# Kernel optimization log

Measured on AMD Instinct MI355X. Metric: run time of the kernel, lower is better.

The kernel has to match this reference:

```python
import jax, jax.numpy as jnp
import numpy as np

N_NODES = 50000
N_EDGES = 800000
IN_DIM = 128
HID = 128
N_LAYERS = 2


def setup_inputs() -> dict:
    key = jax.random.key(0)
    ks = jax.random.split(key, 16)
    x = jax.random.normal(ks[0], (N_NODES, IN_DIM), dtype=jnp.float32)
    edge_index = jax.random.randint(ks[1], (2, N_EDGES), 0, N_NODES, dtype=jnp.int64)
    def lin(k, fan_in, fan_out):
        bound = 1.0 / np.sqrt(fan_in)
        k1, k2 = jax.random.split(k)
        W = jax.random.uniform(k1, (fan_in, fan_out), jnp.float32, -bound, bound)
        b = jax.random.uniform(k2, (fan_out,), jnp.float32, -bound, bound)
        return W, b
    W1_0, b1_0 = lin(ks[2], IN_DIM, HID)
    W2_0, b2_0 = lin(ks[3], HID, HID)
    W1_1, b1_1 = lin(ks[4], HID, HID)
    W2_1, b2_1 = lin(ks[5], HID, HID)
    Wr, br = lin(ks[6], HID, 1)
    return dict(x=x, edge_index=edge_index,
                W1_0=W1_0, b1_0=b1_0, W2_0=W2_0, b2_0=b2_0,
                W1_1=W1_1, b1_1=b1_1, W2_1=W2_1, b2_1=b2_1,
                Wr=Wr, br=br)


def _gin_conv(x, src, dst, W1, b1, W2, b2):
    # GINConv (eps=0): h = MLP(x + sum_{j in N(i)} x_j)
    msgs = x[src]                                   # [E, d] gather
    agg = jax.ops.segment_sum(msgs, dst, num_segments=x.shape[0])  # [N, d] scatter-add
    h = x + agg
    h = jax.nn.relu(h @ W1 + b1)
    return h @ W2 + b2


def reference(x, edge_index, W1_0, b1_0, W2_0, b2_0, W1_1, b1_1, W2_1, b2_1, Wr, br):
    src, dst = edge_index[0], edge_index[1]
    # layer 0
    h = jax.nn.relu(_gin_conv(x, src, dst, W1_0, b1_0, W2_0, b2_0))
    # layer 1 (dropout is identity in eval mode)
    h = jax.nn.relu(_gin_conv(h, src, dst, W1_1, b1_1, W2_1, b2_1))
    return h @ Wr + br
```

## Files before the change

kernel.cpp:

```cpp
#include <hip/hip_runtime.h>

#define HIDDEN 128
#define NB_SHIFT 7
#define NPB 128
#define EPB 4096

typedef __attribute__((ext_vector_type(8))) short short8;
typedef __attribute__((ext_vector_type(4))) float f32x4;
typedef _Float16 f16;
typedef __attribute__((ext_vector_type(8))) _Float16 f16x8;

__device__ __forceinline__ ushort f2bf(float a) {
  union { float f; unsigned u; } c; c.f = a;
  return (ushort)((c.u + 0x7FFFu + ((c.u >> 16) & 1u)) >> 16);
}
__device__ __forceinline__ float bf2f(ushort h) {
  union { unsigned u; float f; } c; c.u = ((unsigned)h) << 16;
  return c.f;
}

__global__ __launch_bounds__(256) void bucket_hist_kernel(
    const int* __restrict__ dst, int* __restrict__ bcnt, int E, int NB) {
  __shared__ int loc[512];
  const int t = threadIdx.x;
  loc[t] = 0; loc[t + 256] = 0;
  __syncthreads();
  const int base = blockIdx.x * EPB;
  const int end = min(base + EPB, E);
  for (int e = base + t; e < end; e += 256)
    atomicAdd(&loc[dst[e] >> NB_SHIFT], 1);
  __syncthreads();
  for (int b = t; b < NB; b += 256)
    if (loc[b]) atomicAdd(&bcnt[b], loc[b]);
}

__global__ __launch_bounds__(256) void scan_buckets_kernel(
    const int* __restrict__ bcnt, int* __restrict__ pairOff,
    int* __restrict__ gCursor, int NB) {
  __shared__ int sh[512];
  const int t = threadIdx.x;
  const int v0 = (t < NB) ? bcnt[t] : 0;
  const int v1 = (t + 256 < NB) ? bcnt[t + 256] : 0;
  sh[t] = v0; sh[t + 256] = v1;
  __syncthreads();
#pragma unroll
  for (int off = 1; off < 512; off <<= 1) {
    int a = (t >= off) ? sh[t - off] : 0;
    int b = (t + 256 >= off) ? sh[t + 256 - off] : 0;
    __syncthreads();
    sh[t] += a; sh[t + 256] += b;
    __syncthreads();
  }
  const int e0 = sh[t] - v0;
  const int e1 = sh[t + 256] - v1;
  pairOff[t] = e0; gCursor[t] = e0;
  pairOff[t + 256] = e1; gCursor[t + 256] = e1;
  if (t == 255) pairOff[512] = sh[511];
}

__global__ __launch_bounds__(256) void partition_kernel(
    const int* __restrict__ src, const int* __restrict__ dst,
    int* __restrict__ gCursor, int* __restrict__ pairs, int E, int NB) {
  __shared__ int loc[512];
  __shared__ int cur[512];
  const int t = threadIdx.x;
  loc[t] = 0; loc[t + 256] = 0;
  __syncthreads();
  const int base = blockIdx.x * EPB;
  const int end = min(base + EPB, E);
  for (int e = base + t; e < end; e += 256)
    atomicAdd(&loc[dst[e] >> NB_SHIFT], 1);
  __syncthreads();
  for (int b = t; b < NB; b += 256)
    cur[b] = loc[b] ? atomicAdd(&gCursor[b], loc[b]) : 0;
  __syncthreads();
  for (int e = base + t; e < end; e += 256) {
    const int d = dst[e];
    const int p = atomicAdd(&cur[d >> NB_SHIFT], 1);
    pairs[p] = ((d & (NPB - 1)) << 25) | src[e];
  }
}

__global__ __launch_bounds__(256) void build_csr_kernel(
    const int* __restrict__ pairs, const int* __restrict__ pairOff,
    int* __restrict__ rowptr, int* __restrict__ col, int M, int E, int NB) {
  __shared__ int deg[NPB];
  __shared__ int pre[NPB];
  __shared__ int cur[NPB];
  const int b = blockIdx.x;
  const int t = threadIdx.x;
  const int s = pairOff[b];
  const int e2 = pairOff[b + 1];
  const int nodeBase = b << NB_SHIFT;
  const int nNodes = min(NPB, M - nodeBase);
  if (t < NPB) deg[t] = 0;
  __syncthreads();
  for (int i = s + t; i < e2; i += 256)
    atomicAdd(&deg[((unsigned)pairs[i]) >> 25], 1);
  __syncthreads();
  if (t < NPB) pre[t] = deg[t];
  __syncthreads();
#pragma unroll
  for (int off = 1; off < NPB; off <<= 1) {
    int v = (t < NPB && t >= off) ? pre[t - off] : 0;
    __syncthreads();
    if (t < NPB) pre[t] += v;
    __syncthreads();
  }
  if (t < nNodes) rowptr[nodeBase + t] = s + pre[t] - deg[t];
  if (b == NB - 1 && t == 0) rowptr[M] = E;
  if (t < NPB) cur[t] = pre[t] - deg[t];
  __syncthreads();
  for (int i = s + t; i < e2; i += 256) {
    const int pr = pairs[i];
    const int pos = s + atomicAdd(&cur[((unsigned)pr) >> 25], 1);
    col[pos] = pr & 0x1FFFFFF;
  }
}

__global__ __launch_bounds__(256) void f2h_kernel(const float* __restrict__ in,
                                                  f16* __restrict__ out, int n8) {
  int i = blockIdx.x * 256 + threadIdx.x;
  if (i >= n8) return;
  const float4* p = (const float4*)(in + (size_t)i * 8);
  float4 a = p[0], b = p[1];
  f16x8 o;
  o[0] = (f16)a.x; o[1] = (f16)a.y; o[2] = (f16)a.z; o[3] = (f16)a.w;
  o[4] = (f16)b.x; o[5] = (f16)b.y; o[6] = (f16)b.z; o[7] = (f16)b.w;
  *(f16x8*)(out + (size_t)i * 8) = o;
}

__global__ __launch_bounds__(256) void prepack_kernel(
    const float* __restrict__ Wa, const float* __restrict__ Wb,
    const float* __restrict__ Wc, const float* __restrict__ Wd,
    ushort* __restrict__ out) {
  int idx = blockIdx.x * 256 + threadIdx.x;
  int w = idx >> 11;
  int rem = idx & 2047;
  int ks = rem >> 9;
  int nf = (rem >> 6) & 7;
  int lane = rem & 63;
  const float* W = (w == 0) ? Wa : (w == 1) ? Wb : (w == 2) ? Wc : Wd;
  const int kbase = ks * 32 + (lane >> 4) * 8;
  const int n = nf * 16 + (lane & 15);
  ushort* oh = out + (size_t)w * 32768 + (size_t)rem * 8;
  ushort* ol = oh + 16384;
#pragma unroll
  for (int j = 0; j < 8; ++j) {
    float v = W[(size_t)(kbase + j) * HIDDEN + n];
    ushort h = f2bf(v);
    oh[j] = h;
    ol[j] = f2bf(v - bf2f(h));
  }
}

__global__ __launch_bounds__(256, 4) void gin_layer_kernel(
    const f16* __restrict__ xh, const int* __restrict__ rowptr,
    const int* __restrict__ col, const ushort* __restrict__ W1p,
    const float* __restrict__ b1, const ushort* __restrict__ W2p,
    const float* __restrict__ b2, f16* __restrict__ Ch,
    const float* __restrict__ Wr, const float* __restrict__ br,
    float* __restrict__ outv, int M, int doReadout) {
  __shared__ float h1[4][16][133];
  const int t = threadIdx.x;
  const int lane = t & 63;
  const int w = t >> 6;
  const int r = lane & 15;
  const int g = lane >> 4;
  const int mBase = blockIdx.x * 64 + w * 16;
  int arow = mBase + r;
  if (arow > M - 1) arow = M - 1;

  float a32[4][8];
  {
    const f16* rp = xh + (size_t)arow * HIDDEN + g * 8;
    f16x8 s0 = *(const f16x8*)(rp);
    f16x8 s1 = *(const f16x8*)(rp + 32);
    f16x8 s2 = *(const f16x8*)(rp + 64);
    f16x8 s3 = *(const f16x8*)(rp + 96);
#pragma unroll
    for (int j = 0; j < 8; ++j) {
      a32[0][j] = (float)s0[j]; a32[1][j] = (float)s1[j];
      a32[2][j] = (float)s2[j]; a32[3][j] = (float)s3[j];
    }
    const int s = rowptr[arow];
    const int e = rowptr[arow + 1];
    int i = s;
    for (; i + 3 < e; i += 4) {
      const int c0 = col[i], c1 = col[i + 1], c2 = col[i + 2], c3 = col[i + 3];
      const f16* p0 = xh + (size_t)c0 * HIDDEN + g * 8;
      const f16* p1 = xh + (size_t)c1 * HIDDEN + g * 8;
      const f16* p2 = xh + (size_t)c2 * HIDDEN + g * 8;
      const f16* p3 = xh + (size_t)c3 * HIDDEN + g * 8;
      f16x8 u0 = *(const f16x8*)(p0);
      f16x8 u1 = *(const f16x8*)(p0 + 32);
      f16x8 u2 = *(const f16x8*)(p0 + 64);
      f16x8 u3 = *(const f16x8*)(p0 + 96);
      f16x8 v0 = *(const f16x8*)(p1);
      f16x8 v1 = *(const f16x8*)(p1 + 32);
      f16x8 v2 = *(const f16x8*)(p1 + 64);
      f16x8 v3 = *(const f16x8*)(p1 + 96);
      f16x8 w0 = *(const f16x8*)(p2);
      f16x8 w1 = *(const f16x8*)(p2 + 32);
      f16x8 w2 = *(const f16x8*)(p2 + 64);
      f16x8 w3 = *(const f16x8*)(p2 + 96);
      f16x8 x0 = *(const f16x8*)(p3);
      f16x8 x1 = *(const f16x8*)(p3 + 32);
      f16x8 x2 = *(const f16x8*)(p3 + 64);
      f16x8 x3 = *(const f16x8*)(p3 + 96);
#pragma unroll
      for (int j = 0; j < 8; ++j) {
        a32[0][j] += ((float)u0[j] + (float)v0[j]) + ((float)w0[j] + (float)x0[j]);
        a32[1][j] += ((float)u1[j] + (float)v1[j]) + ((float)w1[j] + (float)x1[j]);
        a32[2][j] += ((float)u2[j] + (float)v2[j]) + ((float)w2[j] + (float)x2[j]);
        a32[3][j] += ((float)u3[j] + (float)v3[j]) + ((float)w3[j] + (float)x3[j]);
      }
    }
    for (; i < e; ++i) {
      const int c0 = col[i];
      const f16* p0 = xh + (size_t)c0 * HIDDEN + g * 8;
      f16x8 u0 = *(const f16x8*)(p0);
      f16x8 u1 = *(const f16x8*)(p0 + 32);
      f16x8 u2 = *(const f16x8*)(p0 + 64);
      f16x8 u3 = *(const f16x8*)(p0 + 96);
#pragma unroll
      for (int j = 0; j < 8; ++j) {
        a32[0][j] += (float)u0[j];
        a32[1][j] += (float)u1[j];
        a32[2][j] += (float)u2[j];
        a32[3][j] += (float)u3[j];
      }
    }
  }

  f32x4 acc[8];
#pragma unroll
  for (int i = 0; i < 8; ++i) acc[i] = (f32x4){0.f, 0.f, 0.f, 0.f};

#pragma unroll
  for (int ks = 0; ks < 4; ++ks) {
    short8 ah, al;
#pragma unroll
    for (int j = 0; j < 8; ++j) {
      ushort h = f2bf(a32[ks][j]);
      ah[j] = (short)h;
      al[j] = (short)f2bf(a32[ks][j] - bf2f(h));
    }
#pragma unroll
    for (int nf = 0; nf < 8; ++nf) {
      const ushort* bp = W1p + ((size_t)(ks * 8 + nf) * 64 + lane) * 8;
      short8 bh = *(const short8*)bp;
      short8 bl = *(const short8*)(bp + 16384);
      acc[nf] = __builtin_amdgcn_mfma_f32_16x16x32_bf16(ah, bh, acc[nf], 0, 0, 0);
      acc[nf] = __builtin_amdgcn_mfma_f32_16x16x32_bf16(al, bh, acc[nf], 0, 0, 0);
      acc[nf] = __builtin_amdgcn_mfma_f32_16x16x32_bf16(ah, bl, acc[nf], 0, 0, 0);
    }
  }

#pragma unroll
  for (int nf = 0; nf < 8; ++nf) {
    float bv = b1[nf * 16 + r];
#pragma unroll
    for (int q = 0; q < 4; ++q)
      h1[w][g * 4 + q][nf * 16 + r] = fmaxf(acc[nf][q] + bv, 0.f);
    acc[nf] = (f32x4){0.f, 0.f, 0.f, 0.f};
  }

#pragma unroll
  for (int ks = 0; ks < 4; ++ks) {
    const float* hp = &h1[w][r][ks * 32 + g * 8];
    float4 a0 = *(const float4*)hp;
    float4 a1 = *(const float4*)(hp + 4);
    float av[8] = {a0.x, a0.y, a0.z, a0.w, a1.x, a1.y, a1.z, a1.w};
    short8 ah, al;
#pragma unroll
    for (int j = 0; j < 8; ++j) {
      ushort h = f2bf(av[j]);
      ah[j] = (short)h;
      al[j] = (short)f2bf(av[j] - bf2f(h));
    }
#pragma unroll
    for (int nf = 0; nf < 8; ++nf) {
      const ushort* bp = W2p + ((size_t)(ks * 8 + nf) * 64 + lane) * 8;
      short8 bh = *(const short8*)bp;
      short8 bl = *(const short8*)(bp + 16384);
      acc[nf] = __builtin_amdgcn_mfma_f32_16x16x32_bf16(ah, bh, acc[nf], 0, 0, 0);
      acc[nf] = __builtin_amdgcn_mfma_f32_16x16x32_bf16(al, bh, acc[nf], 0, 0, 0);
      acc[nf] = __builtin_amdgcn_mfma_f32_16x16x32_bf16(ah, bl, acc[nf], 0, 0, 0);
    }
  }

  if (!doReadout) {
#pragma unroll
    for (int nf = 0; nf < 8; ++nf) {
      float bv = b2[nf * 16 + r];
#pragma unroll
      for (int q = 0; q < 4; ++q)
        h1[w][g * 4 + q][nf * 16 + r] = fmaxf(acc[nf][q] + bv, 0.f);
    }
    const int rr = lane >> 2;
    const int c0 = (lane & 3) * 32;
    const int gm = mBase + rr;
    if (gm < M) {
#pragma unroll
      for (int i = 0; i < 4; ++i) {
        float4 v0 = *(const float4*)&h1[w][rr][c0 + i * 8];
        float4 v1 = *(const float4*)&h1[w][rr][c0 + i * 8 + 4];
        f16x8 o;
        o[0] = (f16)v0.x; o[1] = (f16)v0.y; o[2] = (f16)v0.z; o[3] = (f16)v0.w;
        o[4] = (f16)v1.x; o[5] = (f16)v1.y; o[6] = (f16)v1.z; o[7] = (f16)v1.w;
        *(f16x8*)(Ch + (size_t)gm * HIDDEN + c0 + i * 8) = o;
      }
    }
  } else {
    float p[4] = {0.f, 0.f, 0.f, 0.f};
#pragma unroll
    for (int nf = 0; nf < 8; ++nf) {
      float bv = b2[nf * 16 + r];
      float wv = Wr[nf * 16 + r];
#pragma unroll
      for (int q = 0; q < 4; ++q) {
        float h = fmaxf(acc[nf][q] + bv, 0.f);
        p[q] += h * wv;
      }
    }
#pragma unroll
    for (int q = 0; q < 4; ++q) {
      p[q] += __shfl_xor(p[q], 8);
      p[q] += __shfl_xor(p[q], 4);
      p[q] += __shfl_xor(p[q], 2);
      p[q] += __shfl_xor(p[q], 1);
    }
    if (r == 0) {
      float brv = br[0];
#pragma unroll
      for (int q = 0; q < 4; ++q) {
        int gm = mBase + g * 4 + q;
        if (gm < M) outv[gm] = p[q] + brv;
      }
    }
  }
}

extern "C" void kernel_launch(void* const* d_in, const int* in_sizes, int n_in,
                              void* d_out, int out_size, void* d_ws,
                              size_t ws_size, hipStream_t stream) {
  const float* x = (const float*)d_in[0];
  const int* ei = (const int*)d_in[1];
  const float* W1_0 = (const float*)d_in[2];
  const float* b1_0 = (const float*)d_in[3];
  const float* W2_0 = (const float*)d_in[4];
  const float* b2_0 = (const float*)d_in[5];
  const float* W1_1 = (const float*)d_in[6];
  const float* b1_1 = (const float*)d_in[7];
  const float* W2_1 = (const float*)d_in[8];
  const float* b2_1 = (const float*)d_in[9];
  const float* Wr = (const float*)d_in[10];
  const float* br = (const float*)d_in[11];

  const int M = in_sizes[0] / HIDDEN;
  const int E = in_sizes[1] / 2;
  const int* src = ei;
  const int* dst = ei + E;
  const int NB = (M + NPB - 1) >> NB_SHIFT;

  int* pairs = (int*)d_ws;
  f16* xh = (f16*)(pairs + E);
  f16* Bh = xh + (size_t)M * HIDDEN;
  int* rowptr = (int*)(Bh + (size_t)M * HIDDEN);
  int* col = rowptr + M + 1;
  int* bcnt = col + E;
  int* pairOff = bcnt + 512;
  int* gCursor = pairOff + 513;
  ushort* Wpk = (ushort*)(gCursor + 512);

  const int ginBlocks = (M + 63) / 64;
  const int cvtBlocks = (M * 16 + 255) / 256;
  const int edgeBlocks = (E + EPB - 1) / EPB;
  float* out = (float*)d_out;

  prepack_kernel<<<32, 256, 0, stream>>>(W1_0, W2_0, W1_1, W2_1, Wpk);
  f2h_kernel<<<cvtBlocks, 256, 0, stream>>>(x, xh, M * 16);

  hipMemsetAsync(bcnt, 0, 512 * sizeof(int), stream);
  bucket_hist_kernel<<<edgeBlocks, 256, 0, stream>>>(dst, bcnt, E, NB);
  scan_buckets_kernel<<<1, 256, 0, stream>>>(bcnt, pairOff, gCursor, NB);
  partition_kernel<<<edgeBlocks, 256, 0, stream>>>(src, dst, gCursor, pairs,
                                                   E, NB);
  build_csr_kernel<<<NB, 256, 0, stream>>>(pairs, pairOff, rowptr, col, M, E,
                                           NB);

  gin_layer_kernel<<<ginBlocks, 256, 0, stream>>>(
      xh, rowptr, col, Wpk, b1_0, Wpk + 32768, b2_0, Bh,
      nullptr, nullptr, nullptr, M, 0);

  gin_layer_kernel<<<ginBlocks, 256, 0, stream>>>(
      Bh, rowptr, col, Wpk + 65536, b1_1, Wpk + 98304, b2_1, nullptr,
      Wr, br, out, M, 1);
}
```

Measured before the change: 254.7 us.

## Split each node's neighbor gather and MLP output columns across two waves

Each block now handles 16 nodes with two wavefronts. Each wave gathers half of every node's neighbor list, the partial sums are combined through shared memory, and each wave then computes half of the output columns of both MLP matmuls. The goal is shorter per-wave gather latency chains and more parallelism in the memory-bound aggregation. The cost is extra syncthreads, LDS exchange traffic, and a cross-wave reduction for the readout.

```diff
diff --git a/kernel.cpp b/kernel.cpp
--- a/kernel.cpp
+++ b/kernel.cpp
@@ -154,25 +154,26 @@
   }
 }
 
-__global__ __launch_bounds__(256, 4) void gin_layer_kernel(
+__global__ __launch_bounds__(128, 6) void gin_layer_kernel(
     const f16* __restrict__ xh, const int* __restrict__ rowptr,
     const int* __restrict__ col, const ushort* __restrict__ W1p,
     const float* __restrict__ b1, const ushort* __restrict__ W2p,
     const float* __restrict__ b2, f16* __restrict__ Ch,
     const float* __restrict__ Wr, const float* __restrict__ br,
     float* __restrict__ outv, int M, int doReadout) {
-  __shared__ float h1[4][16][133];
+  __shared__ float buf[16][132];
+  __shared__ float pr[16];
   const int t = threadIdx.x;
   const int lane = t & 63;
-  const int w = t >> 6;
+  const int h = t >> 6;
   const int r = lane & 15;
   const int g = lane >> 4;
-  const int mBase = blockIdx.x * 64 + w * 16;
+  const int mBase = blockIdx.x * 16;
   int arow = mBase + r;
   if (arow > M - 1) arow = M - 1;
 
   float a32[4][8];
-  {
+  if (h == 0) {
     const f16* rp = xh + (size_t)arow * HIDDEN + g * 8;
     f16x8 s0 = *(const f16x8*)(rp);
     f16x8 s1 = *(const f16x8*)(rp + 32);
@@ -183,8 +184,18 @@
       a32[0][j] = (float)s0[j]; a32[1][j] = (float)s1[j];
       a32[2][j] = (float)s2[j]; a32[3][j] = (float)s3[j];
     }
-    const int s = rowptr[arow];
-    const int e = rowptr[arow + 1];
+  } else {
+#pragma unroll
+    for (int ks = 0; ks < 4; ++ks)
+#pragma unroll
+      for (int j = 0; j < 8; ++j) a32[ks][j] = 0.f;
+  }
+  {
+    const int sAll = rowptr[arow];
+    const int eAll = rowptr[arow + 1];
+    const int mid = sAll + ((eAll - sAll) >> 1);
+    const int s = h ? mid : sAll;
+    const int e = h ? eAll : mid;
     int i = s;
     for (; i + 3 < e; i += 4) {
       const int c0 = col[i], c1 = col[i + 1], c2 = col[i + 2], c3 = col[i + 3];
@@ -233,95 +244,142 @@
     }
   }
 
-  f32x4 acc[8];
-#pragma unroll
-  for (int i = 0; i < 8; ++i) acc[i] = (f32x4){0.f, 0.f, 0.f, 0.f};
+  if (h == 1) {
+#pragma unroll
+    for (int ks = 0; ks < 4; ++ks) {
+      *(float4*)&buf[r][ks * 32 + g * 8] =
+          make_float4(a32[ks][0], a32[ks][1], a32[ks][2], a32[ks][3]);
+      *(float4*)&buf[r][ks * 32 + g * 8 + 4] =
+          make_float4(a32[ks][4], a32[ks][5], a32[ks][6], a32[ks][7]);
+    }
+  }
+  __syncthreads();
+  if (h == 0) {
+#pragma unroll
+    for (int ks = 0; ks < 4; ++ks) {
+      float4 q0 = *(const float4*)&buf[r][ks * 32 + g * 8];
+      float4 q1 = *(const float4*)&buf[r][ks * 32 + g * 8 + 4];
+      a32[ks][0] += q0.x; a32[ks][1] += q0.y; a32[ks][2] += q0.z; a32[ks][3] += q0.w;
+      a32[ks][4] += q1.x; a32[ks][5] += q1.y; a32[ks][6] += q1.z; a32[ks][7] += q1.w;
+    }
+  }
+  __syncthreads();
+  if (h == 0) {
+#pragma unroll
+    for (int ks = 0; ks < 4; ++ks) {
+      *(float4*)&buf[r][ks * 32 + g * 8] =
+          make_float4(a32[ks][0], a32[ks][1], a32[ks][2], a32[ks][3]);
+      *(float4*)&buf[r][ks * 32 + g * 8 + 4] =
+          make_float4(a32[ks][4], a32[ks][5], a32[ks][6], a32[ks][7]);
+    }
+  }
+  __syncthreads();
+  if (h == 1) {
+#pragma unroll
+    for (int ks = 0; ks < 4; ++ks) {
+      float4 q0 = *(const float4*)&buf[r][ks * 32 + g * 8];
+      float4 q1 = *(const float4*)&buf[r][ks * 32 + g * 8 + 4];
+      a32[ks][0] = q0.x; a32[ks][1] = q0.y; a32[ks][2] = q0.z; a32[ks][3] = q0.w;
+      a32[ks][4] = q1.x; a32[ks][5] = q1.y; a32[ks][6] = q1.z; a32[ks][7] = q1.w;
+    }
+  }
+  __syncthreads();
+
+  f32x4 acc[4];
+#pragma unroll
+  for (int i = 0; i < 4; ++i) acc[i] = (f32x4){0.f, 0.f, 0.f, 0.f};
 
 #pragma unroll
   for (int ks = 0; ks < 4; ++ks) {
     short8 ah, al;
 #pragma unroll
     for (int j = 0; j < 8; ++j) {
-      ushort h = f2bf(a32[ks][j]);
-      ah[j] = (short)h;
-      al[j] = (short)f2bf(a32[ks][j] - bf2f(h));
-    }
-#pragma unroll
-    for (int nf = 0; nf < 8; ++nf) {
-      const ushort* bp = W1p + ((size_t)(ks * 8 + nf) * 64 + lane) * 8;
+      ushort hh = f2bf(a32[ks][j]);
+      ah[j] = (short)hh;
+      al[j] = (short)f2bf(a32[ks][j] - bf2f(hh));
+    }
+#pragma unroll
+    for (int nfi = 0; nfi < 4; ++nfi) {
+      const ushort* bp = W1p + ((size_t)(ks * 8 + h * 4 + nfi) * 64 + lane) * 8;
       short8 bh = *(const short8*)bp;
       short8 bl = *(const short8*)(bp + 16384);
-      acc[nf] = __builtin_amdgcn_mfma_f32_16x16x32_bf16(ah, bh, acc[nf], 0, 0, 0);
-      acc[nf] = __builtin_amdgcn_mfma_f32_16x16x32_bf16(al, bh, acc[nf], 0, 0, 0);
-      acc[nf] = __builtin_amdgcn_mfma_f32_16x16x32_bf16(ah, bl, acc[nf], 0, 0, 0);
-    }
-  }
-
-#pragma unroll
-  for (int nf = 0; nf < 8; ++nf) {
+      acc[nfi] = __builtin_amdgcn_mfma_f32_16x16x32_bf16(ah, bh, acc[nfi], 0, 0, 0);
+      acc[nfi] = __builtin_amdgcn_mfma_f32_16x16x32_bf16(al, bh, acc[nfi], 0, 0, 0);
+      acc[nfi] = __builtin_amdgcn_mfma_f32_16x16x32_bf16(ah, bl, acc[nfi], 0, 0, 0);
+    }
+  }
+
+#pragma unroll
+  for (int nfi = 0; nfi < 4; ++nfi) {
+    const int nf = h * 4 + nfi;
     float bv = b1[nf * 16 + r];
 #pragma unroll
     for (int q = 0; q < 4; ++q)
-      h1[w][g * 4 + q][nf * 16 + r] = fmaxf(acc[nf][q] + bv, 0.f);
-    acc[nf] = (f32x4){0.f, 0.f, 0.f, 0.f};
-  }
+      buf[g * 4 + q][nf * 16 + r] = fmaxf(acc[nfi][q] + bv, 0.f);
+    acc[nfi] = (f32x4){0.f, 0.f, 0.f, 0.f};
+  }
+  __syncthreads();
 
 #pragma unroll
   for (int ks = 0; ks < 4; ++ks) {
-    const float* hp = &h1[w][r][ks * 32 + g * 8];
+    const float* hp = &buf[r][ks * 32 + g * 8];
     float4 a0 = *(const float4*)hp;
     float4 a1 = *(const float4*)(hp + 4);
     float av[8] = {a0.x, a0.y, a0.z, a0.w, a1.x, a1.y, a1.z, a1.w};
     short8 ah, al;
 #pragma unroll
     for (int j = 0; j < 8; ++j) {
-      ushort h = f2bf(av[j]);
-      ah[j] = (short)h;
-      al[j] = (short)f2bf(av[j] - bf2f(h));
-    }
-#pragma unroll
-    for (int nf = 0; nf < 8; ++nf) {
-      const ushort* bp = W2p + ((size_t)(ks * 8 + nf) * 64 + lane) * 8;
+      ushort hh = f2bf(av[j]);
+      ah[j] = (short)hh;
+      al[j] = (short)f2bf(av[j] - bf2f(hh));
+    }
+#pragma unroll
+    for (int nfi = 0; nfi < 4; ++nfi) {
+      const ushort* bp = W2p + ((size_t)(ks * 8 + h * 4 + nfi) * 64 + lane) * 8;
       short8 bh = *(const short8*)bp;
       short8 bl = *(const short8*)(bp + 16384);
-      acc[nf] = __builtin_amdgcn_mfma_f32_16x16x32_bf16(ah, bh, acc[nf], 0, 0, 0);
-      acc[nf] = __builtin_amdgcn_mfma_f32_16x16x32_bf16(al, bh, acc[nf], 0, 0, 0);
-      acc[nf] = __builtin_amdgcn_mfma_f32_16x16x32_bf16(ah, bl, acc[nf], 0, 0, 0);
+      acc[nfi] = __builtin_amdgcn_mfma_f32_16x16x32_bf16(ah, bh, acc[nfi], 0, 0, 0);
+      acc[nfi] = __builtin_amdgcn_mfma_f32_16x16x32_bf16(al, bh, acc[nfi], 0, 0, 0);
+      acc[nfi] = __builtin_amdgcn_mfma_f32_16x16x32_bf16(ah, bl, acc[nfi], 0, 0, 0);
     }
   }
 
   if (!doReadout) {
-#pragma unroll
-    for (int nf = 0; nf < 8; ++nf) {
+    __syncthreads();
+#pragma unroll
+    for (int nfi = 0; nfi < 4; ++nfi) {
+      const int nf = h * 4 + nfi;
       float bv = b2[nf * 16 + r];
 #pragma unroll
       for (int q = 0; q < 4; ++q)
-        h1[w][g * 4 + q][nf * 16 + r] = fmaxf(acc[nf][q] + bv, 0.f);
-    }
-    const int rr = lane >> 2;
-    const int c0 = (lane & 3) * 32;
+        buf[g * 4 + q][nf * 16 + r] = fmaxf(acc[nfi][q] + bv, 0.f);
+    }
+    __syncthreads();
+    const int rr = t >> 3;
     const int gm = mBase + rr;
     if (gm < M) {
 #pragma unroll
-      for (int i = 0; i < 4; ++i) {
-        float4 v0 = *(const float4*)&h1[w][rr][c0 + i * 8];
-        float4 v1 = *(const float4*)&h1[w][rr][c0 + i * 8 + 4];
+      for (int i = 0; i < 2; ++i) {
+        const int c0 = (t & 7) * 8 + i * 64;
+        float4 v0 = *(const float4*)&buf[rr][c0];
+        float4 v1 = *(const float4*)&buf[rr][c0 + 4];
         f16x8 o;
         o[0] = (f16)v0.x; o[1] = (f16)v0.y; o[2] = (f16)v0.z; o[3] = (f16)v0.w;
         o[4] = (f16)v1.x; o[5] = (f16)v1.y; o[6] = (f16)v1.z; o[7] = (f16)v1.w;
-        *(f16x8*)(Ch + (size_t)gm * HIDDEN + c0 + i * 8) = o;
+        *(f16x8*)(Ch + (size_t)gm * HIDDEN + c0) = o;
       }
     }
   } else {
     float p[4] = {0.f, 0.f, 0.f, 0.f};
 #pragma unroll
-    for (int nf = 0; nf < 8; ++nf) {
+    for (int nfi = 0; nfi < 4; ++nfi) {
+      const int nf = h * 4 + nfi;
       float bv = b2[nf * 16 + r];
       float wv = Wr[nf * 16 + r];
 #pragma unroll
       for (int q = 0; q < 4; ++q) {
-        float h = fmaxf(acc[nf][q] + bv, 0.f);
-        p[q] += h * wv;
+        float hv = fmaxf(acc[nfi][q] + bv, 0.f);
+        p[q] += hv * wv;
       }
     }
 #pragma unroll
@@ -331,12 +389,17 @@
       p[q] += __shfl_xor(p[q], 2);
       p[q] += __shfl_xor(p[q], 1);
     }
-    if (r == 0) {
+    if (h == 1 && r == 0) {
+#pragma unroll
+      for (int q = 0; q < 4; ++q) pr[g * 4 + q] = p[q];
+    }
+    __syncthreads();
+    if (h == 0 && r == 0) {
       float brv = br[0];
 #pragma unroll
       for (int q = 0; q < 4; ++q) {
         int gm = mBase + g * 4 + q;
-        if (gm < M) outv[gm] = p[q] + brv;
+        if (gm < M) outv[gm] = p[q] + pr[g * 4 + q] + brv;
       }
     }
   }
@@ -374,7 +437,7 @@
   int* gCursor = pairOff + 513;
   ushort* Wpk = (ushort*)(gCursor + 512);
 
-  const int ginBlocks = (M + 63) / 64;
+  const int ginBlocks = (M + 15) / 16;
   const int cvtBlocks = (M * 16 + 255) / 256;
   const int edgeBlocks = (E + EPB - 1) / EPB;
   float* out = (float*)d_out;
@@ -390,11 +453,11 @@
   build_csr_kernel<<<NB, 256, 0, stream>>>(pairs, pairOff, rowptr, col, M, E,
                                            NB);
 
-  gin_layer_kernel<<<ginBlocks, 256, 0, stream>>>(
+  gin_layer_kernel<<<ginBlocks, 128, 0, stream>>>(
       xh, rowptr, col, Wpk, b1_0, Wpk + 32768, b2_0, Bh,
       nullptr, nullptr, nullptr, M, 0);
 
-  gin_layer_kernel<<<ginBlocks, 256, 0, stream>>>(
+  gin_layer_kernel<<<ginBlocks, 128, 0, stream>>>(
       Bh, rowptr, col, Wpk + 65536, b1_1, Wpk + 98304, b2_1, nullptr,
       Wr, br, out, M, 1);
 }
```

New measurement: 384.6 us. +51.0%, slower.
